# Kernel optimization log

Measured on AMD Instinct MI355X. Metric: run time of the kernel, lower is better.

## Reference

```python
import jax, jax.numpy as jnp
import numpy as np

B, QDIM, KDIM, EMBED, HEADS = 8, 256, 256, 512, 8
HIMG, WIMG = 32, 32
HEAD_DIM = EMBED // HEADS


def setup_inputs() -> dict:
    key = jax.random.key(0)
    ks = jax.random.split(key, 8)
    scale_q = 1.0 / np.sqrt(QDIM)
    scale_k = 1.0 / np.sqrt(KDIM)
    return {
        "query": jax.random.normal(ks[0], (B, QDIM, HIMG, WIMG), jnp.float32),
        "key": jax.random.normal(ks[1], (B, KDIM, HIMG, WIMG), jnp.float32),
        "Wq": jax.random.uniform(ks[2], (EMBED, QDIM), jnp.float32, -scale_q, scale_q),
        "bq": jax.random.uniform(ks[3], (EMBED,), jnp.float32, -scale_q, scale_q),
        "Wk": jax.random.uniform(ks[4], (EMBED, KDIM), jnp.float32, -scale_k, scale_k),
        "bk": jax.random.uniform(ks[5], (EMBED,), jnp.float32, -scale_k, scale_k),
        "Wv": jax.random.uniform(ks[6], (EMBED, KDIM), jnp.float32, -scale_k, scale_k),
        "bv": jax.random.uniform(ks[7], (EMBED,), jnp.float32, -scale_k, scale_k),
    }


def reference(query, key, Wq, bq, Wk, bk, Wv, bv):
    b, _, h, w = query.shape
    s = h * w
    # (B, C, H, W) -> (B, S, C)
    q = query.transpose(0, 2, 3, 1).reshape(b, s, QDIM)
    kv = key.transpose(0, 2, 3, 1).reshape(b, s, KDIM)
    q = q @ Wq.T + bq            # (B, S, E)
    k = kv @ Wk.T + bk
    v = kv @ Wv.T + bv
    # split heads: (B, S, H, D) -> (B, H, S, D)
    q = q.reshape(b, s, HEADS, HEAD_DIM).transpose(0, 2, 1, 3)
    k = k.reshape(b, s, HEADS, HEAD_DIM).transpose(0, 2, 1, 3)
    v = v.reshape(b, s, HEADS, HEAD_DIM).transpose(0, 2, 1, 3)
    scores = jnp.einsum("bhqd,bhkd->bhqk", q, k) / np.sqrt(HEAD_DIM)
    # causal additive mask: -inf above the diagonal
    causal = jnp.tril(jnp.ones((s, s), dtype=bool))
    scores = jnp.where(causal, scores, -jnp.inf)
    attn = jax.nn.softmax(scores, axis=-1)
    x = jnp.einsum("bhqk,bhkd->bhqd", attn, v)   # (B, H, S, D)
    # (B, H, S, D) -> (B, H, D, S) -> (B, E, H_img, W_img)
    out = x.transpose(0, 1, 3, 2).reshape(b, EMBED, h, w)
    return out
```

## Files before the change

kernel.cpp:

```cpp
#include <hip/hip_runtime.h>
#include <hip/hip_bf16.h>

#define BATCH 8
#define CDIM 256
#define SEQ 1024
#define EMB 512
#define NHEAD 8
#define HDIM 64

typedef __bf16 bf16x8 __attribute__((ext_vector_type(8)));
typedef float f32x4 __attribute__((ext_vector_type(4)));
typedef float f32x16 __attribute__((ext_vector_type(16)));

static __device__ __forceinline__ unsigned short f2b(float f) {
    __hip_bfloat16 h = __float2bfloat16(f);
    return __builtin_bit_cast(unsigned short, h);
}

static __device__ __forceinline__ f32x4 mfma16(bf16x8 a, bf16x8 b, f32x4 c) {
    return __builtin_amdgcn_mfma_f32_16x16x32_bf16(a, b, c, 0, 0, 0);
}
static __device__ __forceinline__ f32x16 mfma32(bf16x8 a, bf16x8 b, f32x16 c) {
    return __builtin_amdgcn_mfma_f32_32x32x16_bf16(a, b, c, 0, 0, 0);
}

static __device__ __forceinline__ void gload16(const void* g, void* l) {
    __builtin_amdgcn_global_load_lds(
        (const __attribute__((address_space(1))) unsigned int*)g,
        (__attribute__((address_space(3))) unsigned int*)l, 16, 0, 0);
}


__global__ __launch_bounds__(256) void prep_kernel(
    const float* __restrict__ query, const float* __restrict__ key_,
    const float* __restrict__ Wq, const float* __restrict__ Wk,
    const float* __restrict__ Wv,
    unsigned short* __restrict__ Xq, unsigned short* __restrict__ Xk,
    unsigned short* __restrict__ Wc)
{
    int tid = threadIdx.x;
    int z = blockIdx.z;
    if (z >= 16) {
        int pz = z - 16;
        const float* W = (pz == 0) ? Wq : (pz == 1 ? Wk : Wv);
        int lin = blockIdx.y * 16 + blockIdx.x;
        int idx = (lin * 256 + tid) * 8;
        int e7 = (idx >> 8) & 7;
        float4 v0 = *(const float4*)&W[idx];
        float4 v1 = *(const float4*)&W[idx + 4];
        int4 pk;
        pk.x = (int)((unsigned)f2b(v0.x) | ((unsigned)f2b(v0.y) << 16));
        pk.y = (int)((unsigned)f2b(v0.z) | ((unsigned)f2b(v0.w) << 16));
        pk.z = (int)((unsigned)f2b(v1.x) | ((unsigned)f2b(v1.y) << 16));
        pk.w = (int)((unsigned)f2b(v1.z) | ((unsigned)f2b(v1.w) << 16));
        int dsti = (idx & ~255) | ((idx & 255) ^ (e7 << 3));
        *(int4*)&Wc[(size_t)pz * (EMB * CDIM) + dsti] = pk;
        return;
    }
    __shared__ alignas(16) unsigned short sT[64 * 66];
    int s0 = blockIdx.x * 64, c0 = blockIdx.y * 64;
    int which = z >> 3, b = z & 7;
    const float* src = which ? key_ : query;
    unsigned short* dst = which ? Xk : Xq;

#pragma unroll
    for (int p = 0; p < 4; ++p) {
        int c = (tid >> 4) + p * 16;
        int sch = tid & 15;
        float4 v = *(const float4*)&src[((size_t)b * CDIM + c0 + c) * SEQ + s0 + sch * 4];
        sT[c * 66 + sch * 4 + 0] = f2b(v.x);
        sT[c * 66 + sch * 4 + 1] = f2b(v.y);
        sT[c * 66 + sch * 4 + 2] = f2b(v.z);
        sT[c * 66 + sch * 4 + 3] = f2b(v.w);
    }
    __syncthreads();
#pragma unroll
    for (int p = 0; p < 4; ++p) {
        int s = (tid >> 4) + p * 16;
        int cch = tid & 15;
        unsigned short e0 = sT[(cch * 4 + 0) * 66 + s];
        unsigned short e1 = sT[(cch * 4 + 1) * 66 + s];
        unsigned short e2 = sT[(cch * 4 + 2) * 66 + s];
        unsigned short e3 = sT[(cch * 4 + 3) * 66 + s];
        uint2 pk;
        pk.x = (unsigned)e0 | ((unsigned)e1 << 16);
        pk.y = (unsigned)e2 | ((unsigned)e3 << 16);
        int col = (cch * 4) ^ ((s & 7) << 3);
        *(uint2*)&dst[((size_t)b * SEQ + s0 + s) * CDIM + c0 + col] = pk;
    }
}

__global__ __launch_bounds__(256) void proj_kernel(
    const unsigned short* __restrict__ Xq, const unsigned short* __restrict__ Xk,
    const unsigned short* __restrict__ Wc,
    const float* __restrict__ bq, const float* __restrict__ bk,
    const float* __restrict__ bv,
    unsigned short* __restrict__ Qf, unsigned short* __restrict__ Kf,
    unsigned short* __restrict__ Vf)
{
    __shared__ alignas(16) unsigned short sX[128 * 64];
    __shared__ alignas(16) unsigned short sW[128 * 64];
    int tid = threadIdx.x;
    int n0 = blockIdx.x * 128;
    int m0 = blockIdx.y * 128;
    int proj = n0 >> 9;
    const unsigned short* X = (proj == 0) ? Xq : Xk;
    const float* bias = (proj == 0) ? bq : (proj == 1 ? bk : bv);

    int lane = tid & 63, w = tid >> 6;
    int l16 = lane & 15, lhi = lane >> 4;
    int wr = w >> 1, wc = w & 1;
    int lrow = lane >> 3, lcb = (lane & 7) * 8;

    f32x4 zero = {0.f, 0.f, 0.f, 0.f};
    f32x4 acc[4][4];
#pragma unroll
    for (int i = 0; i < 4; ++i)
#pragma unroll
        for (int j = 0; j < 4; ++j) acc[i][j] = zero;

    for (int kt = 0; kt < 4; ++kt) {
        int c0 = kt * 64;
        if (kt) __syncthreads();
#pragma unroll
        for (int i = 0; i < 4; ++i) {
            int seg = i * 4 + w;
            int row = seg * 8 + lrow;
            gload16(&X[(size_t)(m0 + row) * CDIM + c0 + lcb], &sX[seg * 512]);
            gload16(&Wc[(size_t)(n0 + row) * CDIM + c0 + lcb], &sW[seg * 512]);
        }
        __syncthreads();
        const unsigned short* tA = (proj == 2) ? &sX[0] : &sW[0];
        const unsigned short* tB = (proj == 2) ? &sW[0] : &sX[0];
#pragma unroll
        for (int kk = 0; kk < 2; ++kk) {
            bf16x8 af[4], bfr[4];
#pragma unroll
            for (int i = 0; i < 4; ++i) {
                int r = wr * 64 + i * 16 + l16;
                af[i] = *(const bf16x8*)&tA[r * 64 + ((kk * 32 + lhi * 8) ^ ((r & 7) << 3))];
            }
#pragma unroll
            for (int j = 0; j < 4; ++j) {
                int r = wc * 64 + j * 16 + l16;
                bfr[j] = *(const bf16x8*)&tB[r * 64 + ((kk * 32 + lhi * 8) ^ ((r & 7) << 3))];
            }
#pragma unroll
            for (int i = 0; i < 4; ++i)
#pragma unroll
                for (int j = 0; j < 4; ++j)
                    acc[i][j] = mfma16(af[i], bfr[j], acc[i][j]);
        }
    }

    if (proj != 2) {
        unsigned short* dst = proj ? Kf : Qf;
        float scale = proj ? 1.0f : (0.125f * 1.44269504f);
#pragma unroll
        for (int i = 0; i < 4; ++i) {
            int e0 = (n0 & 511) + wr * 64 + i * 16 + lhi * 4;
            float4 bv4 = *(const float4*)&bias[e0];
            int hh = e0 >> 6, dd = e0 & 63;
            int dblk = dd >> 4, hib = (dd >> 3) & 1, jb = dd & 7;
#pragma unroll
            for (int j = 0; j < 4; ++j) {
                int mg = m0 + wc * 64 + j * 16 + l16;
                int bb = mg >> 10, s = mg & 1023;
                int bh = bb * NHEAD + hh;
                size_t idx = ((size_t)((bh * 32 + (s >> 5)) * 4 + dblk)) * 512 +
                             ((s & 31) + 32 * hib) * 8 + jb;
                uint2 pk;
                pk.x = (unsigned)f2b((acc[i][j][0] + bv4.x) * scale) |
                       ((unsigned)f2b((acc[i][j][1] + bv4.y) * scale) << 16);
                pk.y = (unsigned)f2b((acc[i][j][2] + bv4.z) * scale) |
                       ((unsigned)f2b((acc[i][j][3] + bv4.w) * scale) << 16);
                *(uint2*)&dst[idx] = pk;
            }
        }
    } else {
#pragma unroll
        for (int j = 0; j < 4; ++j) {
            int e = (n0 & 511) + wc * 64 + j * 16 + l16;
            float bval = bias[e];
            int hh = e >> 6, dd = e & 63;
            int t2 = dd >> 5, lr = dd & 31;
#pragma unroll
            for (int i = 0; i < 4; ++i) {
                int mg = m0 + wr * 64 + i * 16 + lhi * 4;
                int bb = mg >> 10, s = mg & 1023;
                int bh = bb * NHEAD + hh;
                int sub = t2 * 2 + ((s >> 4) & 1);
                size_t idx = ((size_t)((bh * 32 + (s >> 5)) * 4 + sub)) * 512 +
                             (lr + 32 * ((s >> 3) & 1)) * 8 + (s & 7);
                uint2 pk;
                pk.x = (unsigned)f2b(acc[i][j][0] + bval) |
                       ((unsigned)f2b(acc[i][j][1] + bval) << 16);
                pk.y = (unsigned)f2b(acc[i][j][2] + bval) |
                       ((unsigned)f2b(acc[i][j][3] + bval) << 16);
                *(uint2*)&Vf[idx] = pk;
            }
        }
    }
}

__global__ __launch_bounds__(64, 3) void attn_kernel(
    const unsigned short* __restrict__ Qf, const unsigned short* __restrict__ Kf,
    const unsigned short* __restrict__ Vf, float* __restrict__ out)
{
    int lane = threadIdx.x;
    int l32 = lane & 31, hi = lane >> 5;
    int bh = blockIdx.x;
    int qt = (int)(gridDim.y - 1 - blockIdx.y);
    int b = bh >> 3, h = bh & 7;
    int q0 = qt * 32;

    const unsigned short* Qs = Qf + ((size_t)(bh * 32 + qt)) * 2048;
    const unsigned short* Khd = Kf + (size_t)bh * 32 * 2048;
    const unsigned short* Vhd = Vf + (size_t)bh * 32 * 2048;

    bf16x8 qf[4];
#pragma unroll
    for (int d = 0; d < 4; ++d)
        qf[d] = *(const bf16x8*)&Qs[d * 512 + lane * 8];

    f32x16 o0, o1;
#pragma unroll
    for (int r = 0; r < 16; ++r) { o0[r] = 0.f; o1[r] = 0.f; }
    float m = -1e30f, l = 0.f;

    bf16x8 kA[8], vv[8];

    auto loadK64 = [&](int kt) {
#pragma unroll
        for (int h2 = 0; h2 < 2; ++h2)
#pragma unroll
            for (int d = 0; d < 4; ++d)
                kA[h2 * 4 + d] = *(const bf16x8*)
                    &Khd[(size_t)(kt + h2) * 2048 + d * 512 + lane * 8];
    };
    auto loadK32 = [&](int kt) {
#pragma unroll
        for (int d = 0; d < 4; ++d)
            kA[d] = *(const bf16x8*)&Khd[(size_t)kt * 2048 + d * 512 + lane * 8];
    };
    auto loadV64 = [&](int kt) {
#pragma unroll
        for (int t2 = 0; t2 < 2; ++t2)
#pragma unroll
            for (int kk = 0; kk < 2; ++kk) {
                vv[t2 * 4 + kk] = *(const bf16x8*)
                    &Vhd[(size_t)kt * 2048 + (t2 * 2 + kk) * 512 + lane * 8];
                vv[t2 * 4 + 2 + kk] = *(const bf16x8*)
                    &Vhd[(size_t)(kt + 1) * 2048 + (t2 * 2 + kk) * 512 + lane * 8];
            }
    };
    auto loadV32 = [&](int kt) {
#pragma unroll
        for (int t2 = 0; t2 < 2; ++t2)
#pragma unroll
            for (int kk = 0; kk < 2; ++kk)
                vv[t2 * 4 + kk] = *(const bf16x8*)
                    &Vhd[(size_t)kt * 2048 + (t2 * 2 + kk) * 512 + lane * 8];
    };
    auto packP = [&](const f32x16& st, bf16x8& pbA, bf16x8& pbB) {
        unsigned u[8];
#pragma unroll
        for (int i = 0; i < 8; ++i) {
            unsigned r_;
            asm("v_cvt_pk_bf16_f32 %0, %1, %2" : "=v"(r_) : "v"(st[2 * i]), "v"(st[2 * i + 1]));
            u[i] = r_;
        }
        asm("v_permlane32_swap_b32 %0, %1" : "+v"(u[0]), "+v"(u[2]));
        asm("v_permlane32_swap_b32 %0, %1" : "+v"(u[1]), "+v"(u[3]));
        asm("v_permlane32_swap_b32 %0, %1" : "+v"(u[4]), "+v"(u[6]));
        asm("v_permlane32_swap_b32 %0, %1" : "+v"(u[5]), "+v"(u[7]));
        uint4 w0 = {u[0], u[1], u[2], u[3]};
        uint4 w1 = {u[4], u[5], u[6], u[7]};
        pbA = __builtin_bit_cast(bf16x8, w0);
        pbB = __builtin_bit_cast(bf16x8, w1);
    };

    auto tile64 = [&](bool maskDiag) {
        f32x16 st0, st1;
#pragma unroll
        for (int r = 0; r < 16; ++r) { st0[r] = 0.f; st1[r] = 0.f; }
        __builtin_amdgcn_s_setprio(1);
#pragma unroll
        for (int d = 0; d < 4; ++d) st0 = mfma32(kA[d], qf[d], st0);
#pragma unroll
        for (int d = 0; d < 4; ++d) st1 = mfma32(kA[4 + d], qf[d], st1);
        __builtin_amdgcn_s_setprio(0);
        if (maskDiag) {
#pragma unroll
            for (int r = 0; r < 16; ++r) {
                int cd = (r & 3) + 8 * (r >> 2) + 4 * hi;
                if (cd > l32) st1[r] = -1e38f;
            }
        }
        float t16[16];
#pragma unroll
        for (int r = 0; r < 16; ++r) t16[r] = fmaxf(st0[r], st1[r]);
        float t8[8];
#pragma unroll
        for (int r = 0; r < 8; ++r) t8[r] = fmaxf(t16[r], t16[r + 8]);
        float t4[4];
#pragma unroll
        for (int r = 0; r < 4; ++r) t4[r] = fmaxf(t8[r], t8[r + 4]);
        float tmax = fmaxf(fmaxf(t4[0], t4[2]), fmaxf(t4[1], t4[3]));
        tmax = fmaxf(tmax, __shfl_xor(tmax, 32));
        if (!__all(tmax <= m + 8.0f)) {
            float mnew = fmaxf(m, tmax);
            float corr = __builtin_amdgcn_exp2f(m - mnew);
#pragma unroll
            for (int r = 0; r < 16; ++r) { o0[r] *= corr; o1[r] *= corr; }
            l *= corr;
            m = mnew;
        }
#pragma unroll
        for (int r = 0; r < 16; ++r) {
            st0[r] = __builtin_amdgcn_exp2f(st0[r] - m);
            st1[r] = __builtin_amdgcn_exp2f(st1[r] - m);
        }
        float s16[16];
#pragma unroll
        for (int r = 0; r < 16; ++r) s16[r] = st0[r] + st1[r];
        float s8[8];
#pragma unroll
        for (int r = 0; r < 8; ++r) s8[r] = s16[r] + s16[r + 8];
        float s4[4];
#pragma unroll
        for (int r = 0; r < 4; ++r) s4[r] = s8[r] + s8[r + 4];
        float ts = (s4[0] + s4[2]) + (s4[1] + s4[3]);
        ts += __shfl_xor(ts, 32);
        l += ts;
        bf16x8 pb0, pb1, pb2, pb3;
        packP(st0, pb0, pb1);
        packP(st1, pb2, pb3);
        __builtin_amdgcn_s_setprio(1);
        o0 = mfma32(vv[0], pb0, o0); o1 = mfma32(vv[4], pb0, o1);
        o0 = mfma32(vv[1], pb1, o0); o1 = mfma32(vv[5], pb1, o1);
        o0 = mfma32(vv[2], pb2, o0); o1 = mfma32(vv[6], pb2, o1);
        o0 = mfma32(vv[3], pb3, o0); o1 = mfma32(vv[7], pb3, o1);
        __builtin_amdgcn_s_setprio(0);
    };

    auto tile32 = [&](bool mask) {
        f32x16 st0;
#pragma unroll
        for (int r = 0; r < 16; ++r) st0[r] = 0.f;
        __builtin_amdgcn_s_setprio(1);
#pragma unroll
        for (int d = 0; d < 4; ++d) st0 = mfma32(kA[d], qf[d], st0);
        __builtin_amdgcn_s_setprio(0);
        if (mask) {
#pragma unroll
            for (int r = 0; r < 16; ++r) {
                int cd = (r & 3) + 8 * (r >> 2) + 4 * hi;
                if (cd > l32) st0[r] = -1e38f;
            }
        }
        float t8[8];
#pragma unroll
        for (int r = 0; r < 8; ++r) t8[r] = fmaxf(st0[r], st0[r + 8]);
        float t4[4];
#pragma unroll
        for (int r = 0; r < 4; ++r) t4[r] = fmaxf(t8[r], t8[r + 4]);
        float tmax = fmaxf(fmaxf(t4[0], t4[2]), fmaxf(t4[1], t4[3]));
        tmax = fmaxf(tmax, __shfl_xor(tmax, 32));
        if (!__all(tmax <= m + 8.0f)) {
            float mnew = fmaxf(m, tmax);
            float corr = __builtin_amdgcn_exp2f(m - mnew);
#pragma unroll
            for (int r = 0; r < 16; ++r) { o0[r] *= corr; o1[r] *= corr; }
            l *= corr;
            m = mnew;
        }
#pragma unroll
        for (int r = 0; r < 16; ++r) st0[r] = __builtin_amdgcn_exp2f(st0[r] - m);
        float s8[8];
#pragma unroll
        for (int r = 0; r < 8; ++r) s8[r] = st0[r] + st0[r + 8];
        float s4[4];
#pragma unroll
        for (int r = 0; r < 4; ++r) s4[r] = s8[r] + s8[r + 4];
        float ts = (s4[0] + s4[2]) + (s4[1] + s4[3]);
        ts += __shfl_xor(ts, 32);
        l += ts;
        bf16x8 pb0, pb1;
        packP(st0, pb0, pb1);
        __builtin_amdgcn_s_setprio(1);
        o0 = mfma32(vv[0], pb0, o0); o0 = mfma32(vv[1], pb1, o0);
        o1 = mfma32(vv[4], pb0, o1); o1 = mfma32(vv[5], pb1, o1);
        __builtin_amdgcn_s_setprio(0);
    };

    int nt64 = (qt + 1) >> 1;
    bool tail = ((qt & 1) == 0);
    for (int t = 0; t < nt64; ++t) {
        loadK64(2 * t);
        loadV64(2 * t);
        tile64((t == nt64 - 1) && !tail);
    }
    if (tail) {
        loadK32(qt);
        loadV32(qt);
        tile32(true);
    }

    float inv = 1.0f / l;
    size_t base = ((size_t)b * EMB + h * HDIM) * SEQ + q0 + l32;
#pragma unroll
    for (int r = 0; r < 16; ++r) {
        int d0 = (r & 3) + 8 * (r >> 2) + 4 * hi;
        out[base + (size_t)d0 * SEQ] = o0[r] * inv;
        out[base + (size_t)(d0 + 32) * SEQ] = o1[r] * inv;
    }
}

extern "C" void kernel_launch(void* const* d_in, const int* in_sizes, int n_in,
                              void* d_out, int out_size, void* d_ws, size_t ws_size,
                              hipStream_t stream) {
    const float* query = (const float*)d_in[0];
    const float* key_  = (const float*)d_in[1];
    const float* Wq    = (const float*)d_in[2];
    const float* bq    = (const float*)d_in[3];
    const float* Wk    = (const float*)d_in[4];
    const float* bk    = (const float*)d_in[5];
    const float* Wv    = (const float*)d_in[6];
    const float* bv    = (const float*)d_in[7];
    float* out = (float*)d_out;

    char* ws = (char*)d_ws;
    unsigned short* Qf = (unsigned short*)(ws);
    unsigned short* Kf = (unsigned short*)(ws + 8388608);
    unsigned short* Vf = (unsigned short*)(ws + 16777216);
    unsigned short* Xq = (unsigned short*)(ws + 25165824);
    unsigned short* Xk = (unsigned short*)(ws + 29360128);
    unsigned short* Wc = (unsigned short*)((char*)d_out + 16777216 - 1048576);

    prep_kernel<<<dim3(16, 4, 19), 256, 0, stream>>>(query, key_, Wq, Wk, Wv, Xq, Xk, Wc);
    proj_kernel<<<dim3(12, 64), 256, 0, stream>>>(Xq, Xk, Wc, bq, bk, bv, Qf, Kf, Vf);
    attn_kernel<<<dim3(BATCH * NHEAD, SEQ / 32), 64, 0, stream>>>(Qf, Kf, Vf, out);
}
```

Measured before the change: 118.8 us.

## Split attention key tiles across four waves with LDS softmax merge

Each attention block now runs four wavefronts instead of one. Each wave takes every fourth 32-key tile and keeps its own running max, sum and output accumulator, then writes them to shared memory. Wave 0 combines the four partial results with log-sum-exp rescaling and writes the output. This splits the serial key loop across waves to cut the critical-path latency of the long causal rows. In exchange it adds LDS traffic, a block barrier and a serial merge step, drops the 64-key tile path, and leaves waves idle on short rows.

```diff
diff --git a/kernel.cpp b/kernel.cpp
--- a/kernel.cpp
+++ b/kernel.cpp
@@ -203,11 +203,14 @@
     }
 }
 
-__global__ __launch_bounds__(64, 3) void attn_kernel(
+__global__ __launch_bounds__(256, 3) void attn_kernel(
     const unsigned short* __restrict__ Qf, const unsigned short* __restrict__ Kf,
     const unsigned short* __restrict__ Vf, float* __restrict__ out)
 {
-    int lane = threadIdx.x;
+    __shared__ alignas(16) float sO[4][2][64][17];
+    __shared__ float sM[4][32], sL[4][32];
+    int tid = threadIdx.x;
+    int lane = tid & 63, w = tid >> 6;
     int l32 = lane & 31, hi = lane >> 5;
     int bh = blockIdx.x;
     int qt = (int)(gridDim.y - 1 - blockIdx.y);
@@ -228,40 +231,8 @@
     for (int r = 0; r < 16; ++r) { o0[r] = 0.f; o1[r] = 0.f; }
     float m = -1e30f, l = 0.f;
 
-    bf16x8 kA[8], vv[8];
-
-    auto loadK64 = [&](int kt) {
-#pragma unroll
-        for (int h2 = 0; h2 < 2; ++h2)
-#pragma unroll
-            for (int d = 0; d < 4; ++d)
-                kA[h2 * 4 + d] = *(const bf16x8*)
-                    &Khd[(size_t)(kt + h2) * 2048 + d * 512 + lane * 8];
-    };
-    auto loadK32 = [&](int kt) {
-#pragma unroll
-        for (int d = 0; d < 4; ++d)
-            kA[d] = *(const bf16x8*)&Khd[(size_t)kt * 2048 + d * 512 + lane * 8];
-    };
-    auto loadV64 = [&](int kt) {
-#pragma unroll
-        for (int t2 = 0; t2 < 2; ++t2)
-#pragma unroll
-            for (int kk = 0; kk < 2; ++kk) {
-                vv[t2 * 4 + kk] = *(const bf16x8*)
-                    &Vhd[(size_t)kt * 2048 + (t2 * 2 + kk) * 512 + lane * 8];
-                vv[t2 * 4 + 2 + kk] = *(const bf16x8*)
-                    &Vhd[(size_t)(kt + 1) * 2048 + (t2 * 2 + kk) * 512 + lane * 8];
-            }
-    };
-    auto loadV32 = [&](int kt) {
-#pragma unroll
-        for (int t2 = 0; t2 < 2; ++t2)
-#pragma unroll
-            for (int kk = 0; kk < 2; ++kk)
-                vv[t2 * 4 + kk] = *(const bf16x8*)
-                    &Vhd[(size_t)kt * 2048 + (t2 * 2 + kk) * 512 + lane * 8];
-    };
+    bf16x8 kA[4], vvl[4];
+
     auto packP = [&](const f32x16& st, bf16x8& pbA, bf16x8& pbB) {
         unsigned u[8];
 #pragma unroll
@@ -280,71 +251,17 @@
         pbB = __builtin_bit_cast(bf16x8, w1);
     };
 
-    auto tile64 = [&](bool maskDiag) {
-        f32x16 st0, st1;
-#pragma unroll
-        for (int r = 0; r < 16; ++r) { st0[r] = 0.f; st1[r] = 0.f; }
-        __builtin_amdgcn_s_setprio(1);
-#pragma unroll
-        for (int d = 0; d < 4; ++d) st0 = mfma32(kA[d], qf[d], st0);
-#pragma unroll
-        for (int d = 0; d < 4; ++d) st1 = mfma32(kA[4 + d], qf[d], st1);
-        __builtin_amdgcn_s_setprio(0);
-        if (maskDiag) {
-#pragma unroll
-            for (int r = 0; r < 16; ++r) {
-                int cd = (r & 3) + 8 * (r >> 2) + 4 * hi;
-                if (cd > l32) st1[r] = -1e38f;
-            }
-        }
-        float t16[16];
-#pragma unroll
-        for (int r = 0; r < 16; ++r) t16[r] = fmaxf(st0[r], st1[r]);
-        float t8[8];
-#pragma unroll
-        for (int r = 0; r < 8; ++r) t8[r] = fmaxf(t16[r], t16[r + 8]);
-        float t4[4];
-#pragma unroll
-        for (int r = 0; r < 4; ++r) t4[r] = fmaxf(t8[r], t8[r + 4]);
-        float tmax = fmaxf(fmaxf(t4[0], t4[2]), fmaxf(t4[1], t4[3]));
-        tmax = fmaxf(tmax, __shfl_xor(tmax, 32));
-        if (!__all(tmax <= m + 8.0f)) {
-            float mnew = fmaxf(m, tmax);
-            float corr = __builtin_amdgcn_exp2f(m - mnew);
-#pragma unroll
-            for (int r = 0; r < 16; ++r) { o0[r] *= corr; o1[r] *= corr; }
-            l *= corr;
-            m = mnew;
-        }
-#pragma unroll
-        for (int r = 0; r < 16; ++r) {
-            st0[r] = __builtin_amdgcn_exp2f(st0[r] - m);
-            st1[r] = __builtin_amdgcn_exp2f(st1[r] - m);
-        }
-        float s16[16];
-#pragma unroll
-        for (int r = 0; r < 16; ++r) s16[r] = st0[r] + st1[r];
-        float s8[8];
-#pragma unroll
-        for (int r = 0; r < 8; ++r) s8[r] = s16[r] + s16[r + 8];
-        float s4[4];
-#pragma unroll
-        for (int r = 0; r < 4; ++r) s4[r] = s8[r] + s8[r + 4];
-        float ts = (s4[0] + s4[2]) + (s4[1] + s4[3]);
-        ts += __shfl_xor(ts, 32);
-        l += ts;
-        bf16x8 pb0, pb1, pb2, pb3;
-        packP(st0, pb0, pb1);
-        packP(st1, pb2, pb3);
-        __builtin_amdgcn_s_setprio(1);
-        o0 = mfma32(vv[0], pb0, o0); o1 = mfma32(vv[4], pb0, o1);
-        o0 = mfma32(vv[1], pb1, o0); o1 = mfma32(vv[5], pb1, o1);
-        o0 = mfma32(vv[2], pb2, o0); o1 = mfma32(vv[6], pb2, o1);
-        o0 = mfma32(vv[3], pb3, o0); o1 = mfma32(vv[7], pb3, o1);
-        __builtin_amdgcn_s_setprio(0);
-    };
-
-    auto tile32 = [&](bool mask) {
+    for (int kt = w; kt <= qt; kt += 4) {
+#pragma unroll
+        for (int d = 0; d < 4; ++d)
+            kA[d] = *(const bf16x8*)&Khd[(size_t)kt * 2048 + d * 512 + lane * 8];
+#pragma unroll
+        for (int t2 = 0; t2 < 2; ++t2)
+#pragma unroll
+            for (int kk = 0; kk < 2; ++kk)
+                vvl[t2 * 2 + kk] = *(const bf16x8*)
+                    &Vhd[(size_t)kt * 2048 + (t2 * 2 + kk) * 512 + lane * 8];
+
         f32x16 st0;
 #pragma unroll
         for (int r = 0; r < 16; ++r) st0[r] = 0.f;
@@ -352,7 +269,7 @@
 #pragma unroll
         for (int d = 0; d < 4; ++d) st0 = mfma32(kA[d], qf[d], st0);
         __builtin_amdgcn_s_setprio(0);
-        if (mask) {
+        if (kt == qt) {
 #pragma unroll
             for (int r = 0; r < 16; ++r) {
                 int cd = (r & 3) + 8 * (r >> 2) + 4 * hi;
@@ -389,31 +306,46 @@
         bf16x8 pb0, pb1;
         packP(st0, pb0, pb1);
         __builtin_amdgcn_s_setprio(1);
-        o0 = mfma32(vv[0], pb0, o0); o0 = mfma32(vv[1], pb1, o0);
-        o1 = mfma32(vv[4], pb0, o1); o1 = mfma32(vv[5], pb1, o1);
+        o0 = mfma32(vvl[0], pb0, o0); o0 = mfma32(vvl[1], pb1, o0);
+        o1 = mfma32(vvl[2], pb0, o1); o1 = mfma32(vvl[3], pb1, o1);
         __builtin_amdgcn_s_setprio(0);
-    };
-
-    int nt64 = (qt + 1) >> 1;
-    bool tail = ((qt & 1) == 0);
-    for (int t = 0; t < nt64; ++t) {
-        loadK64(2 * t);
-        loadV64(2 * t);
-        tile64((t == nt64 - 1) && !tail);
-    }
-    if (tail) {
-        loadK32(qt);
-        loadV32(qt);
-        tile32(true);
-    }
-
-    float inv = 1.0f / l;
-    size_t base = ((size_t)b * EMB + h * HDIM) * SEQ + q0 + l32;
-#pragma unroll
-    for (int r = 0; r < 16; ++r) {
-        int d0 = (r & 3) + 8 * (r >> 2) + 4 * hi;
-        out[base + (size_t)d0 * SEQ] = o0[r] * inv;
-        out[base + (size_t)(d0 + 32) * SEQ] = o1[r] * inv;
+    }
+
+#pragma unroll
+    for (int rr = 0; rr < 4; ++rr) {
+        *(float4*)&sO[w][0][lane][rr * 4] =
+            make_float4(o0[rr * 4], o0[rr * 4 + 1], o0[rr * 4 + 2], o0[rr * 4 + 3]);
+        *(float4*)&sO[w][1][lane][rr * 4] =
+            make_float4(o1[rr * 4], o1[rr * 4 + 1], o1[rr * 4 + 2], o1[rr * 4 + 3]);
+    }
+    if (hi == 0) { sM[w][l32] = m; sL[w][l32] = l; }
+    __syncthreads();
+
+    if (w == 0) {
+        float m0_ = sM[0][l32], m1_ = sM[1][l32], m2_ = sM[2][l32], m3_ = sM[3][l32];
+        float mm = fmaxf(fmaxf(m0_, m1_), fmaxf(m2_, m3_));
+        float sc0 = __builtin_amdgcn_exp2f(m0_ - mm);
+        float sc1 = __builtin_amdgcn_exp2f(m1_ - mm);
+        float sc2 = __builtin_amdgcn_exp2f(m2_ - mm);
+        float sc3 = __builtin_amdgcn_exp2f(m3_ - mm);
+        float lsum = sL[0][l32] * sc0 + sL[1][l32] * sc1 +
+                     sL[2][l32] * sc2 + sL[3][l32] * sc3;
+        float inv = 1.0f / lsum;
+        float fo0[16], fo1[16];
+#pragma unroll
+        for (int r = 0; r < 16; ++r) {
+            fo0[r] = sO[0][0][lane][r] * sc0 + sO[1][0][lane][r] * sc1 +
+                     sO[2][0][lane][r] * sc2 + sO[3][0][lane][r] * sc3;
+            fo1[r] = sO[0][1][lane][r] * sc0 + sO[1][1][lane][r] * sc1 +
+                     sO[2][1][lane][r] * sc2 + sO[3][1][lane][r] * sc3;
+        }
+        size_t base = ((size_t)b * EMB + h * HDIM) * SEQ + q0 + l32;
+#pragma unroll
+        for (int r = 0; r < 16; ++r) {
+            int d0 = (r & 3) + 8 * (r >> 2) + 4 * hi;
+            out[base + (size_t)d0 * SEQ] = fo0[r] * inv;
+            out[base + (size_t)(d0 + 32) * SEQ] = fo1[r] * inv;
+        }
     }
 }
 
@@ -440,5 +372,5 @@
 
     prep_kernel<<<dim3(16, 4, 19), 256, 0, stream>>>(query, key_, Wq, Wk, Wv, Xq, Xk, Wc);
     proj_kernel<<<dim3(12, 64), 256, 0, stream>>>(Xq, Xk, Wc, bq, bk, bv, Qf, Kf, Vf);
-    attn_kernel<<<dim3(BATCH * NHEAD, SEQ / 32), 64, 0, stream>>>(Qf, Kf, Vf, out);
-}
+    attn_kernel<<<dim3(BATCH * NHEAD, SEQ / 32), 256, 0, stream>>>(Qf, Kf, Vf, out);
+}
```

New measurement: 116.1 us. -2.3%, faster.
